# Kernel optimization log

Measured on AMD Instinct MI355X. Metric: run time of the kernel, lower is better.

The kernel has to match this reference:

```python
import jax, jax.numpy as jnp
import numpy as np
from jax import lax

B, CIN, H, W = 4, 64, 256, 256
Q, K = 256, 16


def _conv3x3_replicate(x, w, b):
    # replicate (edge) padding of 1, then VALID conv -> same spatial size
    xp = jnp.pad(x, ((0, 0), (0, 0), (1, 1), (1, 1)), mode='edge')
    y = lax.conv_general_dilated(xp, w, (1, 1), 'VALID',
                                 dimension_numbers=('NCHW', 'OIHW', 'NCHW'))
    return y + b[None, :, None, None]


def setup_inputs() -> dict:
    key = jax.random.key(0)
    ks = jax.random.split(key, 9)
    s1 = 1.0 / np.sqrt(CIN * 9)
    s2 = 1.0 / np.sqrt(Q * 9)
    s3 = 1.0 / np.sqrt(Q)
    return {
        'x':  jax.random.normal(ks[0], (B, CIN, H, W), jnp.float32),
        'w1': jax.random.normal(ks[1], (Q, CIN, 3, 3), jnp.float32) * s1,
        'b1': jax.random.normal(ks[2], (Q,), jnp.float32) * s1,
        'w2': jax.random.normal(ks[3], (Q, Q, 3, 3), jnp.float32) * s2,
        'b2': jax.random.normal(ks[4], (Q,), jnp.float32) * s2,
        'w3': jax.random.normal(ks[5], (Q, Q, 1, 1), jnp.float32) * s3,
        'b3': jax.random.normal(ks[6], (Q,), jnp.float32) * s3,
        'mu': jax.random.normal(ks[7], (K, Q), jnp.float32),      # cluster_mu squeezed
        'label': jax.random.normal(ks[8], (K,), jnp.float32),
    }


def reference(x, w1, b1, w2, b2, w3, b3, mu, label):
    # query_encoder: Convx2 (conv3x3 replicate + relu, twice) then 1x1 conv
    q = jax.nn.relu(_conv3x3_replicate(x, w1, b1))
    q = jax.nn.relu(_conv3x3_replicate(q, w2, b2))
    q = jnp.einsum('oc,bchw->bohw', w3[:, :, 0, 0], q) + b3[None, :, None, None]
    # logit[b,k,h,w] = -sum_c (q - mu)^2, via norm expansion (no BxKxCxHxW tensor)
    q2 = jnp.sum(q * q, axis=1, keepdims=True)                   # (B,1,H,W)
    mu2 = jnp.sum(mu * mu, axis=1)                               # (K,)
    cross = jnp.einsum('bchw,kc->bkhw', q, mu)                   # (B,K,H,W)
    logit = -(q2 - 2.0 * cross + mu2[None, :, None, None])
    att = jax.nn.softmax(logit, axis=1)                          # softmax over clusters
    out = jnp.einsum('bkhw,k->bhw', att, label)
    return out[:, None]                                          # (B,1,H,W)
```

## Files before the change

kernel.cpp:

```cpp
#include <hip/hip_runtime.h>

#define BB   4
#define CIN  64
#define HH   256
#define WW   256
#define QQ   256
#define KK   16

typedef _Float16 half8 __attribute__((ext_vector_type(8)));
typedef float   f32x16 __attribute__((ext_vector_type(16)));
typedef unsigned int u32;

#define OFF_W1R   0ull
#define OFF_W2R   294912ull
#define OFF_WMU   1474560ull
#define OFF_LGB   1490944ull
#define OFF_ACT0  1605888ull
#define OFF_ACT1  35160320ull

__device__ __forceinline__ void dma16(const void* g, void* l) {
  __builtin_amdgcn_global_load_lds(
      (const __attribute__((address_space(1))) u32*)g,
      (__attribute__((address_space(3))) u32*)l, 16, 0, 0);
}

__global__ __launch_bounds__(256) void k_prep(
    const float* __restrict__ w1, const float* __restrict__ w2,
    const float* __restrict__ w3, const float* __restrict__ b3,
    const float* __restrict__ mu,
    _Float16* __restrict__ w1r, _Float16* __restrict__ w2r,
    float* __restrict__ wpart, float* __restrict__ lgb) {
  int bid = blockIdx.x, tid = threadIdx.x;
  if (bid < 576) {
    int idx = bid * 256 + tid;
    int blk = idx >> 13;
    int cc = blk / 9, tt = blk - cc * 9;
    int rem = idx & 8191;
    int ks = rem >> 12;
    int n  = (rem >> 4) & 255;
    int kh = (rem >> 3) & 1;
    int e  = rem & 7;
    int c = cc * 32 + ks * 16 + kh * 8 + e;
    w1r[idx] = (_Float16)w1[(n * 64 + c) * 9 + tt];
  } else if (bid < 2880) {
    int d = (bid - 576) * 256 + tid;
    int blk = d >> 13;
    int cc = blk / 9, tt = blk - cc * 9;
    int rem = d & 8191;
    int ks = rem >> 12;
    int n  = (rem >> 4) & 255;
    int kh = (rem >> 3) & 1;
    int e  = rem & 7;
    int c = cc * 32 + ks * 16 + kh * 8 + e;
    w2r[d] = (_Float16)w2[(n * 256 + c) * 9 + tt];
  } else if (bid < 3008) {
    int j = bid - 2880;
    int k = j >> 3, o0 = (j & 7) << 5;
    float s = 0.f;
#pragma unroll 4
    for (int oi = 0; oi < 32; ++oi) {
      int o = o0 + oi;
      s = fmaf(mu[k * 256 + o], w3[o * 256 + tid], s);
    }
    wpart[j * 256 + tid] = s;
  } else {
    int k = bid - 3008;
    float m = mu[k * 256 + tid];
    __shared__ float red[256];
    red[tid] = m * (2.f * b3[tid] - m);
    __syncthreads();
    for (int st = 128; st > 0; st >>= 1) {
      if (tid < st) red[tid] += red[tid + st];
      __syncthreads();
    }
    if (tid == 0) lgb[k] = red[0];
  }
}

__global__ __launch_bounds__(256) void k_prep2(
    const float* __restrict__ wpart, float* __restrict__ wmu2) {
  int k = blockIdx.x, tid = threadIdx.x;
  float s = 0.f;
#pragma unroll
  for (int p = 0; p < 8; ++p) s += wpart[(k * 8 + p) * 256 + tid];
  wmu2[k * 256 + tid] = 2.f * s;
}

__global__ __launch_bounds__(256) void k_t0(const float* __restrict__ x,
                                            _Float16* __restrict__ act0) {
  __shared__ float tile[64][65];
  int blk = blockIdx.x;
  int b = blk >> 10;
  int p0 = (blk & 1023) << 6;
  int t = threadIdx.x;
  {
    int p = t & 63, c0 = t >> 6;
    const float* xb = x + (size_t)b * (CIN * 65536) + p0 + p;
#pragma unroll
    for (int i = 0; i < 16; ++i) {
      int c = c0 + (i << 2);
      tile[c][p] = xb[(size_t)c * 65536];
    }
  }
  __syncthreads();
  {
    _Float16* o = act0 + (size_t)(b * 65536 + p0) * CIN;
#pragma unroll
    for (int uu = 0; uu < 2; ++uu) {
      int u = t + (uu << 8);
      int px = u & 63, oct = u >> 6;
      half8 h;
#pragma unroll
      for (int i = 0; i < 8; ++i) h[i] = (_Float16)tile[oct * 8 + i][px];
      *(half8*)(o + px * CIN + oct * 8) = h;
    }
  }
}

template <int CI>
__global__ __launch_bounds__(256, 2) void k_conv(
    const _Float16* __restrict__ actin, const char* __restrict__ wr,
    const float* __restrict__ bias, _Float16* __restrict__ actout) {
  constexpr int NC = CI / 32;
  constexpr int NT = 9 * NC;
  __shared__ __align__(16) char smem[67584];
  auto As = (char(*)[12288])smem;
  _Float16* Qs = (_Float16*)smem;

  int tid = threadIdx.x;
  int b = blockIdx.x >> 9;
  int tile = blockIdx.x & 511;
  int txi = tile & 15, tyi = tile >> 4;
  int x0 = txi << 4, y0 = tyi << 3;
  int lane = tid & 63, wave = tid >> 6;
  int mwave = wave >> 1, nwave = wave & 1;
  int l31 = lane & 31, khalf = lane >> 5;

  f32x16 acc[2][4];
#pragma unroll
  for (int s = 0; s < 2; ++s)
#pragma unroll
    for (int nt = 0; nt < 4; ++nt)
#pragma unroll
      for (int r = 0; r < 16; ++r) acc[s][nt][r] = 0.f;

  const char* aG[3];
  int aL[3];
#pragma unroll
  for (int i = 0; i < 3; ++i) {
    int px = (wave * 3 + i) * 16 + (lane >> 2);
    int s = lane & 3;
    int pxc = min(px, 179);
    int hy = pxc / 18, hx = pxc - hy * 18;
    int y = min(max(y0 - 1 + hy, 0), 255);
    int x = min(max(x0 - 1 + hx, 0), 255);
    int q = s ^ ((pxc >> 1) & 3);
    aG[i] = (const char*)actin +
            (((size_t)(b * 65536 + y * 256 + x)) * CI + q * 8) * 2;
    aL[i] = (wave * 3 + i) * 1024;
  }

  const char* b0 = wr + ((nwave * 128 + l31) * 32 + khalf * 16);
  const char* b1 = b0 + 8192;

#pragma unroll
  for (int i = 0; i < 3; ++i) dma16(aG[i], &As[0][aL[i]]);

  half8 bf[2][2][4];
#pragma unroll
  for (int nt = 0; nt < 4; ++nt) {
    bf[0][0][nt] = *(const half8*)(b0 + nt * 1024);
    bf[0][1][nt] = *(const half8*)(b1 + nt * 1024);
  }
  b0 += 16384; b1 += 16384;
  asm volatile("s_waitcnt vmcnt(8)" ::: "memory");
  __builtin_amdgcn_s_barrier();

  for (int c2 = 0; c2 < NC; c2 += 2) {
    bool last2 = (c2 + 2 >= NC);
#pragma unroll
    for (int u = 0; u < 18; ++u) {
      int t = (u < 9) ? u : u - 9;
      constexpr int dummy = 0; (void)dummy;
      int pr = u & 1;
      if (u == 6) {
#pragma unroll
        for (int i = 0; i < 3; ++i)
          dma16(aG[i] + (c2 + 1) * 64, &As[1][aL[i]]);
      }
      if (u == 15 && !last2) {
#pragma unroll
        for (int i = 0; i < 3; ++i)
          dma16(aG[i] + (c2 + 2) * 64, &As[0][aL[i]]);
      }
      if (!(last2 && u == 17)) {
#pragma unroll
        for (int nt = 0; nt < 4; ++nt) {
          bf[pr ^ 1][0][nt] = *(const half8*)(b0 + nt * 1024);
          bf[pr ^ 1][1][nt] = *(const half8*)(b1 + nt * 1024);
        }
        b0 += 16384; b1 += 16384;
      }
      const char* Ab = As[(u >= 9) ? 1 : 0];
      int dy = t / 3, dx = t - dy * 3;
      half8 af[2][2];
#pragma unroll
      for (int s = 0; s < 2; ++s) {
        int px = (mwave * 4 + s * 2 + (l31 >> 4) + dy) * 18 + (l31 & 15) + dx;
        int sw = ((px >> 1) & 3) << 4;
#pragma unroll
        for (int ks = 0; ks < 2; ++ks) {
          int q = (ks * 2 + khalf) << 4;
          af[ks][s] = *(const half8*)(Ab + px * 64 + (q ^ sw));
        }
      }
      __builtin_amdgcn_s_setprio(1);
#pragma unroll
      for (int ks = 0; ks < 2; ++ks)
#pragma unroll
        for (int s = 0; s < 2; ++s)
#pragma unroll
          for (int nt = 0; nt < 4; ++nt)
            acc[s][nt] = __builtin_amdgcn_mfma_f32_32x32x16_f16(
                af[ks][s], bf[pr][ks][nt], acc[s][nt], 0, 0, 0);
      __builtin_amdgcn_s_setprio(0);
      if (u == 8) {
        asm volatile("s_waitcnt vmcnt(8) lgkmcnt(0)" ::: "memory");
        __builtin_amdgcn_s_barrier();
      }
      if (u == 17 && !last2) {
        asm volatile("s_waitcnt vmcnt(8) lgkmcnt(0)" ::: "memory");
        __builtin_amdgcn_s_barrier();
      }
    }
  }
  __syncthreads();

#pragma unroll
  for (int s = 0; s < 2; ++s)
#pragma unroll
    for (int nt = 0; nt < 4; ++nt) {
      int n = nwave * 128 + nt * 32 + l31;
      float bn = bias[n];
#pragma unroll
      for (int r = 0; r < 16; ++r) {
        int mrow = (r & 3) + 8 * (r >> 2) + 4 * khalf;
        int p = (mwave * 4 + s * 2 + (mrow >> 4)) * 16 + (mrow & 15);
        Qs[p * 264 + n] = (_Float16)fmaxf(acc[s][nt][r] + bn, 0.f);
      }
    }
  __syncthreads();
  {
    _Float16* gout = actout + (((size_t)(b * 65536 + y0 * 256 + x0)) << 8);
#pragma unroll
    for (int i = 0; i < 16; ++i) {
      int f = tid + (i << 8);
      int p = f >> 5, o = f & 31;
      half8 v = *(const half8*)&Qs[p * 264 + o * 8];
      *(half8*)(gout + (((p >> 4) * 256 + (p & 15)) << 8) + o * 8) = v;
    }
  }
}

__global__ __launch_bounds__(256) void k_head(
    const _Float16* __restrict__ a2_0, const _Float16* __restrict__ a2_1,
    const _Float16* __restrict__ a2_2, const _Float16* __restrict__ a2_3,
    const float* __restrict__ wmu2, const float* __restrict__ lgb,
    const float* __restrict__ label, float* __restrict__ out) {
  int b = blockIdx.x >> 8;
  int px = (blockIdx.x & 255) * 256 + threadIdx.x;
  const _Float16* base = (b == 0) ? a2_0 : (b == 1) ? a2_1
                       : (b == 2) ? a2_2 : a2_3;
  const half8* ap = (const half8*)(base + ((size_t)px << 8));
  float cr[16];
#pragma unroll
  for (int k = 0; k < 16; ++k) cr[k] = lgb[k];
#pragma unroll 2
  for (int cc = 0; cc < 32; ++cc) {
    half8 h = ap[cc];
    float a0 = (float)h[0], a1 = (float)h[1], a2 = (float)h[2],
          a3 = (float)h[3], a4 = (float)h[4], a5 = (float)h[5],
          a6 = (float)h[6], a7 = (float)h[7];
#pragma unroll
    for (int k = 0; k < 16; ++k) {
      const float* w = wmu2 + (k << 8) + (cc << 3);
      float c0 = cr[k];
      c0 = fmaf(a0, w[0], c0);
      c0 = fmaf(a1, w[1], c0);
      c0 = fmaf(a2, w[2], c0);
      c0 = fmaf(a3, w[3], c0);
      c0 = fmaf(a4, w[4], c0);
      c0 = fmaf(a5, w[5], c0);
      c0 = fmaf(a6, w[6], c0);
      c0 = fmaf(a7, w[7], c0);
      cr[k] = c0;
    }
  }
  float mx = cr[0];
#pragma unroll
  for (int k = 1; k < 16; ++k) mx = fmaxf(mx, cr[k]);
  float num = 0.f, den = 0.f;
#pragma unroll
  for (int k = 0; k < 16; ++k) {
    float e = __expf(cr[k] - mx);
    num = fmaf(e, label[k], num);
    den += e;
  }
  out[(size_t)b * 65536 + px] = num / den;
}

extern "C" void kernel_launch(void* const* d_in, const int* in_sizes, int n_in,
                              void* d_out, int out_size, void* d_ws, size_t ws_size,
                              hipStream_t stream) {
  const float* x  = (const float*)d_in[0];
  const float* w1 = (const float*)d_in[1];
  const float* b1 = (const float*)d_in[2];
  const float* w2 = (const float*)d_in[3];
  const float* b2 = (const float*)d_in[4];
  const float* w3 = (const float*)d_in[5];
  const float* b3 = (const float*)d_in[6];
  const float* mu = (const float*)d_in[7];
  const float* label = (const float*)d_in[8];
  float* out = (float*)d_out;

  char* ws = (char*)d_ws;
  _Float16* w1r  = (_Float16*)(ws + OFF_W1R);
  _Float16* w2r  = (_Float16*)(ws + OFF_W2R);
  float*    wmu2 = (float*)   (ws + OFF_WMU);
  float*    lgb  = (float*)   (ws + OFF_LGB);
  _Float16* act0 = (_Float16*)(ws + OFF_ACT0);
  _Float16* act1 = (_Float16*)(ws + OFF_ACT1);
  float*    wpart = (float*)  (ws + OFF_ACT1);

  _Float16* a2d[4] = {
    (_Float16*)(ws + OFF_ACT0),
    act1 + 0 * (size_t)65536 * 256,
    act1 + 1 * (size_t)65536 * 256,
    act1 + 2 * (size_t)65536 * 256
  };

  k_prep<<<3024, 256, 0, stream>>>(w1, w2, w3, b3, mu, w1r, w2r, wpart, lgb);
  k_prep2<<<16, 256, 0, stream>>>(wpart, wmu2);
  k_t0<<<4096, 256, 0, stream>>>(x, act0);
  k_conv<64><<<2048, 256, 0, stream>>>(act0, (const char*)w1r, b1, act1);
  for (int b = 0; b < BB; ++b)
    k_conv<256><<<512, 256, 0, stream>>>(act1 + (size_t)b * 65536 * 256,
                                         (const char*)w2r, b2, a2d[b]);
  k_head<<<1024, 256, 0, stream>>>(a2d[0], a2d[1], a2d[2], a2d[3],
                                   wmu2, lgb, label, out);
}
```

Before: 612.8 us.

## Fuse cluster-attention head into second conv epilogue, drop activation round-trip

The second 3x3 conv kernel now computes the folded 1x1-conv/mu cross terms, softmax over clusters and the label-weighted sum directly from its shared-memory output tile. Two wave halves each reduce half the channels and combine through a shared scratch buffer. This removes the fp16 activation write to global memory and the separate head kernel's reread of it. In exchange, LDS use grows (padded row stride of 272, about 76 KB), which may reduce occupancy, and the epilogue adds FMA work plus an extra barrier in the conv kernel.

```diff
diff --git a/kernel.cpp b/kernel.cpp
--- a/kernel.cpp
+++ b/kernel.cpp
@@ -120,10 +120,14 @@
 template <int CI>
 __global__ __launch_bounds__(256, 2) void k_conv(
     const _Float16* __restrict__ actin, const char* __restrict__ wr,
-    const float* __restrict__ bias, _Float16* __restrict__ actout) {
+    const float* __restrict__ bias, _Float16* __restrict__ actout,
+    const float* __restrict__ wmu2, const float* __restrict__ lgb,
+    const float* __restrict__ label, float* __restrict__ outb) {
   constexpr int NC = CI / 32;
   constexpr int NT = 9 * NC;
-  __shared__ __align__(16) char smem[67584];
+  constexpr int QS = (CI == 256) ? 272 : 264;
+  constexpr int SMEM = (CI == 256) ? 77824 : 67584;
+  __shared__ __align__(16) char smem[SMEM];
   auto As = (char(*)[12288])smem;
   _Float16* Qs = (_Float16*)smem;
 
@@ -181,7 +185,6 @@
 #pragma unroll
     for (int u = 0; u < 18; ++u) {
       int t = (u < 9) ? u : u - 9;
-      constexpr int dummy = 0; (void)dummy;
       int pr = u & 1;
       if (u == 6) {
 #pragma unroll
@@ -246,67 +249,70 @@
       for (int r = 0; r < 16; ++r) {
         int mrow = (r & 3) + 8 * (r >> 2) + 4 * khalf;
         int p = (mwave * 4 + s * 2 + (mrow >> 4)) * 16 + (mrow & 15);
-        Qs[p * 264 + n] = (_Float16)fmaxf(acc[s][nt][r] + bn, 0.f);
+        Qs[p * QS + n] = (_Float16)fmaxf(acc[s][nt][r] + bn, 0.f);
       }
     }
   __syncthreads();
-  {
+
+  if (CI == 64) {
     _Float16* gout = actout + (((size_t)(b * 65536 + y0 * 256 + x0)) << 8);
 #pragma unroll
     for (int i = 0; i < 16; ++i) {
       int f = tid + (i << 8);
       int p = f >> 5, o = f & 31;
-      half8 v = *(const half8*)&Qs[p * 264 + o * 8];
+      half8 v = *(const half8*)&Qs[p * QS + o * 8];
       *(half8*)(gout + (((p >> 4) * 256 + (p & 15)) << 8) + o * 8) = v;
     }
-  }
-}
-
-__global__ __launch_bounds__(256) void k_head(
-    const _Float16* __restrict__ a2_0, const _Float16* __restrict__ a2_1,
-    const _Float16* __restrict__ a2_2, const _Float16* __restrict__ a2_3,
-    const float* __restrict__ wmu2, const float* __restrict__ lgb,
-    const float* __restrict__ label, float* __restrict__ out) {
-  int b = blockIdx.x >> 8;
-  int px = (blockIdx.x & 255) * 256 + threadIdx.x;
-  const _Float16* base = (b == 0) ? a2_0 : (b == 1) ? a2_1
-                       : (b == 2) ? a2_2 : a2_3;
-  const half8* ap = (const half8*)(base + ((size_t)px << 8));
-  float cr[16];
-#pragma unroll
-  for (int k = 0; k < 16; ++k) cr[k] = lgb[k];
+  } else {
+    float* scr = (float*)(smem + 69632);
+    int hf = __builtin_amdgcn_readfirstlane(wave >> 1);
+    int px = ((wave & 1) << 6) + lane;
+    const _Float16* qrow = Qs + px * QS + hf * 128;
+    float cr[16];
+#pragma unroll
+    for (int k = 0; k < 16; ++k) cr[k] = 0.f;
 #pragma unroll 2
-  for (int cc = 0; cc < 32; ++cc) {
-    half8 h = ap[cc];
-    float a0 = (float)h[0], a1 = (float)h[1], a2 = (float)h[2],
-          a3 = (float)h[3], a4 = (float)h[4], a5 = (float)h[5],
-          a6 = (float)h[6], a7 = (float)h[7];
-#pragma unroll
-    for (int k = 0; k < 16; ++k) {
-      const float* w = wmu2 + (k << 8) + (cc << 3);
-      float c0 = cr[k];
-      c0 = fmaf(a0, w[0], c0);
-      c0 = fmaf(a1, w[1], c0);
-      c0 = fmaf(a2, w[2], c0);
-      c0 = fmaf(a3, w[3], c0);
-      c0 = fmaf(a4, w[4], c0);
-      c0 = fmaf(a5, w[5], c0);
-      c0 = fmaf(a6, w[6], c0);
-      c0 = fmaf(a7, w[7], c0);
-      cr[k] = c0;
-    }
-  }
-  float mx = cr[0];
-#pragma unroll
-  for (int k = 1; k < 16; ++k) mx = fmaxf(mx, cr[k]);
-  float num = 0.f, den = 0.f;
-#pragma unroll
-  for (int k = 0; k < 16; ++k) {
-    float e = __expf(cr[k] - mx);
-    num = fmaf(e, label[k], num);
-    den += e;
-  }
-  out[(size_t)b * 65536 + px] = num / den;
+    for (int c8 = 0; c8 < 16; ++c8) {
+      half8 h = *(const half8*)(qrow + c8 * 8);
+      float a0 = (float)h[0], a1 = (float)h[1], a2 = (float)h[2],
+            a3 = (float)h[3], a4 = (float)h[4], a5 = (float)h[5],
+            a6 = (float)h[6], a7 = (float)h[7];
+#pragma unroll
+      for (int k = 0; k < 16; ++k) {
+        const float* w = wmu2 + (k << 8) + (hf << 7) + (c8 << 3);
+        float c0 = cr[k];
+        c0 = fmaf(a0, w[0], c0);
+        c0 = fmaf(a1, w[1], c0);
+        c0 = fmaf(a2, w[2], c0);
+        c0 = fmaf(a3, w[3], c0);
+        c0 = fmaf(a4, w[4], c0);
+        c0 = fmaf(a5, w[5], c0);
+        c0 = fmaf(a6, w[6], c0);
+        c0 = fmaf(a7, w[7], c0);
+        cr[k] = c0;
+      }
+    }
+    if (hf) {
+#pragma unroll
+      for (int k = 0; k < 16; ++k) scr[k * 128 + px] = cr[k];
+    }
+    __syncthreads();
+    if (!hf) {
+#pragma unroll
+      for (int k = 0; k < 16; ++k) cr[k] += scr[k * 128 + px] + lgb[k];
+      float mx = cr[0];
+#pragma unroll
+      for (int k = 1; k < 16; ++k) mx = fmaxf(mx, cr[k]);
+      float num = 0.f, den = 0.f;
+#pragma unroll
+      for (int k = 0; k < 16; ++k) {
+        float e = __expf(cr[k] - mx);
+        num = fmaf(e, label[k], num);
+        den += e;
+      }
+      outb[(y0 + (px >> 4)) * 256 + (x0 + (px & 15))] = num / den;
+    }
+  }
 }
 
 extern "C" void kernel_launch(void* const* d_in, const int* in_sizes, int n_in,
@@ -332,20 +338,14 @@
   _Float16* act1 = (_Float16*)(ws + OFF_ACT1);
   float*    wpart = (float*)  (ws + OFF_ACT1);
 
-  _Float16* a2d[4] = {
-    (_Float16*)(ws + OFF_ACT0),
-    act1 + 0 * (size_t)65536 * 256,
-    act1 + 1 * (size_t)65536 * 256,
-    act1 + 2 * (size_t)65536 * 256
-  };
-
   k_prep<<<3024, 256, 0, stream>>>(w1, w2, w3, b3, mu, w1r, w2r, wpart, lgb);
   k_prep2<<<16, 256, 0, stream>>>(wpart, wmu2);
   k_t0<<<4096, 256, 0, stream>>>(x, act0);
-  k_conv<64><<<2048, 256, 0, stream>>>(act0, (const char*)w1r, b1, act1);
+  k_conv<64><<<2048, 256, 0, stream>>>(act0, (const char*)w1r, b1, act1,
+                                       nullptr, nullptr, nullptr, nullptr);
   for (int b = 0; b < BB; ++b)
     k_conv<256><<<512, 256, 0, stream>>>(act1 + (size_t)b * 65536 * 256,
-                                         (const char*)w2r, b2, a2d[b]);
-  k_head<<<1024, 256, 0, stream>>>(a2d[0], a2d[1], a2d[2], a2d[3],
-                                   wmu2, lgb, label, out);
-}
+                                         (const char*)w2r, b2, nullptr,
+                                         wmu2, lgb, label,
+                                         out + (size_t)b * 65536);
+}
```

Measured after the change: 575.4 us. -6.1%, faster.
